# Kernel tuning notes

Measured on AMD Instinct MI355X. Metric: run time of the kernel, lower is better.

## Reference

```python
import jax, jax.numpy as jnp
import numpy as np

NUM_NODES = 10000  # fixed by input spec: edge_index values in [0, 10000)


def setup_inputs() -> dict:
    key = jax.random.key(0)
    k1, k2, k3 = jax.random.split(key, 3)
    N, E, D_IN, D_OUT = NUM_NODES, 320000, 256, 256
    x = jax.random.normal(k1, (N, D_IN), dtype=jnp.float32)
    edge_index = jax.random.randint(k2, (2, E), 0, N, dtype=jnp.int64)
    # ensure node N-1 appears so num_nodes == N as in the torch code
    edge_index = edge_index.at[0, 0].set(N - 1)
    # xavier_uniform for [D_IN, D_OUT]
    limit = float(np.sqrt(6.0 / (D_IN + D_OUT)))
    weight = jax.random.uniform(k3, (D_IN, D_OUT), dtype=jnp.float32,
                                minval=-limit, maxval=limit)
    return {"x": x, "edge_index": edge_index, "weight": weight}


def _normalize_adjacency(edge_index, num_nodes):
    src, dst = edge_index[0], edge_index[1]
    ones = jnp.ones(src.shape[0], dtype=jnp.float32)
    # symmetric binarized adjacency: adj[i,j] = adj[j,i] = 1 (set, not add)
    adj = jnp.zeros((num_nodes, num_nodes), dtype=jnp.float32)
    adj = adj.at[src, dst].max(ones)
    adj = adj.at[dst, src].max(ones)
    # one round of self-loops: adj += I
    adj = adj + jnp.eye(num_nodes, dtype=jnp.float32)
    deg = jnp.sum(adj, axis=1)                    # [N]
    dinv = 1.0 / jnp.sqrt(deg)                    # [N]
    # D^-1/2 A D^-1/2 via broadcasting (equivalent to diag mms)
    return adj * dinv[:, None] * dinv[None, :]


def reference(x, edge_index, weight):
    adj = _normalize_adjacency(edge_index, NUM_NODES)  # [N, N]
    h = adj @ x                                        # [N, D_IN]
    return h @ weight                                  # [N, D_OUT]
```

## Files before the change

### kernel.cpp

```cpp
#include <hip/hip_runtime.h>
#include <hip/hip_bf16.h>
#include <stdint.h>

#define N_NODES   10000
#define D_FEAT    256
#define E_EDGES   320000
#define ROW_WORDS 313
#define ROW_STRIDE 320
#define LIST_CAP  1024

#define NB     250
#define RPB    40
#define RPC    20
#define S_CAP  48
#define NBLK_E 313
#define NBLK_W 64
#define NBLK_C 500
#define NBLK_G 625
#define COLSTR 128

#define LDSTR 264

typedef __attribute__((ext_vector_type(4))) float float4v;
typedef _Float16 half8  __attribute__((ext_vector_type(8)));
typedef _Float16 half4v __attribute__((ext_vector_type(4)));

__device__ __forceinline__ float h2f_lo(uint32_t u) {
    union { uint32_t u; _Float16 h[2]; } v; v.u = u; return (float)v.h[0];
}
__device__ __forceinline__ float h2f_hi(uint32_t u) {
    union { uint32_t u; _Float16 h[2]; } v; v.u = u; return (float)v.h[1];
}


__global__ void __launch_bounds__(1024)
fill_sort(const int* __restrict__ ei, uint32_t* __restrict__ bucketbuf,
          uint32_t* __restrict__ hist_g,
          const float* __restrict__ w, _Float16* __restrict__ wt) {
    __shared__ uint32_t hist[256];
    __shared__ uint32_t lofs[256];
    __shared__ uint32_t stage[2048];
    __shared__ uint16_t sbkt[2048];
    int t = threadIdx.x;

    if (blockIdx.x >= NBLK_E) {
        int kb = (blockIdx.x - NBLK_E) * 4;
        int k = kb + (t >> 8), n = t & 255;
        float* st = (float*)stage;
        st[(n << 2) | (t >> 8)] = w[(size_t)k * D_FEAT + n];
        __syncthreads();
        if (t < 256) {
            half4v o = { (_Float16)st[t * 4 + 0], (_Float16)st[t * 4 + 1],
                         (_Float16)st[t * 4 + 2], (_Float16)st[t * 4 + 3] };
            *(half4v*)&wt[(size_t)t * D_FEAT + kb] = o;
        }
        return;
    }

    if (t < 256) hist[t] = 0;
    __syncthreads();
    int e = blockIdx.x * 1024 + t;
    int b0 = -1, b1 = -1; uint32_t ent0 = 0, ent1 = 0, s0 = 0, s1 = 0;
    if (e < E_EDGES) {
        int s = ei[e], d = ei[E_EDGES + e];
        if ((uint32_t)s < N_NODES && (uint32_t)d < N_NODES) {
            b0 = s / RPB; ent0 = ((uint32_t)(s - b0 * RPB) << 14) | (uint32_t)d;
            b1 = d / RPB; ent1 = ((uint32_t)(d - b1 * RPB) << 14) | (uint32_t)s;
            s0 = atomicAdd(&hist[b0], 1u);
            s1 = atomicAdd(&hist[b1], 1u);
        }
    }
    __syncthreads();
    if (t < 256) lofs[t] = hist[t];
    __syncthreads();
    for (int d = 1; d < 256; d <<= 1) {
        uint32_t v = 0;
        if (t < 256 && t >= d) v = lofs[t - d];
        __syncthreads();
        if (t < 256) lofs[t] += v;
        __syncthreads();
    }
    if (b0 >= 0) {
        uint32_t p0 = lofs[b0] - hist[b0] + s0;
        stage[p0] = ent0; sbkt[p0] = (uint16_t)b0;
        uint32_t p1 = lofs[b1] - hist[b1] + s1;
        stage[p1] = ent1; sbkt[p1] = (uint16_t)b1;
    }
    __syncthreads();
    uint32_t total = lofs[255];
    uint32_t bb0 = blockIdx.x * 256;
    for (uint32_t idx = t; idx < total; idx += 1024) {
        uint32_t b = sbkt[idx];
        uint32_t pos = idx - (lofs[b] - hist[b]);
        if (pos < S_CAP)
            bucketbuf[(size_t)(bb0 + b) * S_CAP + pos] = stage[idx];
    }
    if (t < 256) hist_g[bb0 + t] = min(hist[t], (uint32_t)S_CAP);
}

__global__ void __launch_bounds__(1024)
csr_gemm(const uint32_t* __restrict__ bucketbuf, const uint32_t* __restrict__ hist_g,
         uint32_t* __restrict__ row_deg, float* __restrict__ dinv,
         uint32_t* __restrict__ col,
         const float* __restrict__ x, const _Float16* __restrict__ wt,
         _Float16* __restrict__ yw) {
    __shared__ __align__(16) uint32_t smem[RPC * ROW_WORDS + NBLK_E];
    int t = threadIdx.x;

    if (blockIdx.x >= NBLK_C) {
        _Float16* a_lds = (_Float16*)smem;
        int r0 = (blockIdx.x - NBLK_C) * 16;
        int row = t >> 6, c4 = (t & 63) * 4;
        float4v xv = *(const float4v*)(x + (size_t)(r0 + row) * D_FEAT + c4);
        half4v h = { (_Float16)xv[0], (_Float16)xv[1],
                     (_Float16)xv[2], (_Float16)xv[3] };
        *(half4v*)&a_lds[row * LDSTR + c4] = h;
        __syncthreads();
        int wv = t >> 6, lane = t & 63;
        int quad = lane >> 4, r = lane & 15;
        int ct = wv;
        const _Float16* pb = wt + (size_t)(ct * 16 + r) * D_FEAT + quad * 8;
        float4v acc = {0.f, 0.f, 0.f, 0.f};
        #pragma unroll
        for (int kk = 0; kk < D_FEAT; kk += 32) {
            half8 a = *(const half8*)&a_lds[r * LDSTR + kk + quad * 8];
            half8 b = *(const half8*)(pb + kk);
            acc = __builtin_amdgcn_mfma_f32_16x16x32_f16(a, b, acc, 0, 0, 0);
        }
        int colg = ct * 16 + r;
        #pragma unroll
        for (int u = 0; u < 4; u++)
            yw[(size_t)(r0 + quad * 4 + u) * D_FEAT + colg] = (_Float16)acc[u];
        return;
    }

    uint32_t* bm       = smem;
    uint32_t* hist_col = smem + RPC * ROW_WORDS;
    int b   = blockIdx.x >> 1;
    int lr0 = (blockIdx.x & 1) * RPC;
    for (int i = t; i < RPC * ROW_WORDS; i += 1024) bm[i] = 0;
    if (t < NBLK_E) hist_col[t] = hist_g[(size_t)t * 256 + b];
    __syncthreads();
    for (int p = t; p < NBLK_E * S_CAP; p += 1024) {
        int sb = p / S_CAP, off = p % S_CAP;
        if ((uint32_t)off < hist_col[sb]) {
            uint32_t ent = bucketbuf[(size_t)(sb * 256 + b) * S_CAP + off];
            uint32_t lr = (ent >> 14) - (uint32_t)lr0;
            if (lr < RPC) {
                uint32_t d = ent & 0x3FFFu;
                atomicOr(&bm[lr * ROW_WORDS + (d >> 5)], 1u << (d & 31));
            }
        }
    }
    __syncthreads();
    int wv = t >> 6, lane = t & 63;
    for (int r = wv; r < RPC; r += 16) {
        int gi = b * RPB + lr0 + r;
        uint32_t wb[5]; int tot = 0;
        #pragma unroll
        for (int k = 0; k < 5; k++) {
            int w = lane + 64 * k;
            uint32_t v = (w < ROW_WORDS) ? bm[r * ROW_WORDS + w] : 0u;
            wb[k] = v; tot += __popc(v);
        }
        int incl = tot;
        #pragma unroll
        for (int off = 1; off < 64; off <<= 1) {
            int v = __shfl_up(incl, off, 64);
            if (lane >= off) incl += v;
        }
        uint32_t total = (uint32_t)__shfl(incl, 63, 64);
        if (lane == 0) {
            row_deg[gi] = min(total, (uint32_t)COLSTR);
            dinv[gi]    = 1.0f / sqrtf((float)(total + 1u));
        }
        uint32_t p = (uint32_t)(incl - tot);
        #pragma unroll
        for (int k = 0; k < 5; k++) {
            uint32_t bits = wb[k];
            uint32_t cbase = (uint32_t)(lane + 64 * k) << 5;
            while (bits) {
                if (p < COLSTR)
                    col[(size_t)gi * COLSTR + p] = cbase + (uint32_t)__builtin_ctz(bits);
                p++;
                bits &= bits - 1;
            }
        }
    }
}

__global__ void __launch_bounds__(256)
spmm_out(const uint32_t* __restrict__ row_deg, const float* __restrict__ dinv,
         const uint32_t* __restrict__ col, const _Float16* __restrict__ ywp,
         float* __restrict__ out) {
    const uint16_t* yw = (const uint16_t*)ywp;
    int wv = threadIdx.x >> 6, lane = threadIdx.x & 63;
    int i = blockIdx.x * 4 + wv;
    uint32_t base = (uint32_t)i * COLSTR;
    uint32_t deg = min(row_deg[i], (uint32_t)COLSTR);
    float di = dinv[i];
    float4v z = {0.f, 0.f, 0.f, 0.f};
    float4v a0 = z, a1 = z, a2 = z, a3 = z, a4 = z, a5 = z, a6 = z, a7 = z;
    size_t ch = (size_t)lane * 4;
    uint32_t t8 = deg & ~7u;
    uint32_t t = 0;
    for (; t < t8; t += 8) {
        uint4 jva = *(const uint4*)&col[base + t];
        uint4 jvb = *(const uint4*)&col[base + t + 4];
        float d0 = dinv[jva.x], d1 = dinv[jva.y], d2 = dinv[jva.z], d3 = dinv[jva.w];
        float d4 = dinv[jvb.x], d5 = dinv[jvb.y], d6 = dinv[jvb.z], d7 = dinv[jvb.w];
        uint2 g0 = *(const uint2*)(yw + (size_t)jva.x * D_FEAT + ch);
        uint2 g1 = *(const uint2*)(yw + (size_t)jva.y * D_FEAT + ch);
        uint2 g2 = *(const uint2*)(yw + (size_t)jva.z * D_FEAT + ch);
        uint2 g3 = *(const uint2*)(yw + (size_t)jva.w * D_FEAT + ch);
        uint2 g4 = *(const uint2*)(yw + (size_t)jvb.x * D_FEAT + ch);
        uint2 g5 = *(const uint2*)(yw + (size_t)jvb.y * D_FEAT + ch);
        uint2 g6 = *(const uint2*)(yw + (size_t)jvb.z * D_FEAT + ch);
        uint2 g7 = *(const uint2*)(yw + (size_t)jvb.w * D_FEAT + ch);
        a0[0] += d0 * h2f_lo(g0.x); a0[1] += d0 * h2f_hi(g0.x);
        a0[2] += d0 * h2f_lo(g0.y); a0[3] += d0 * h2f_hi(g0.y);
        a1[0] += d1 * h2f_lo(g1.x); a1[1] += d1 * h2f_hi(g1.x);
        a1[2] += d1 * h2f_lo(g1.y); a1[3] += d1 * h2f_hi(g1.y);
        a2[0] += d2 * h2f_lo(g2.x); a2[1] += d2 * h2f_hi(g2.x);
        a2[2] += d2 * h2f_lo(g2.y); a2[3] += d2 * h2f_hi(g2.y);
        a3[0] += d3 * h2f_lo(g3.x); a3[1] += d3 * h2f_hi(g3.x);
        a3[2] += d3 * h2f_lo(g3.y); a3[3] += d3 * h2f_hi(g3.y);
        a4[0] += d4 * h2f_lo(g4.x); a4[1] += d4 * h2f_hi(g4.x);
        a4[2] += d4 * h2f_lo(g4.y); a4[3] += d4 * h2f_hi(g4.y);
        a5[0] += d5 * h2f_lo(g5.x); a5[1] += d5 * h2f_hi(g5.x);
        a5[2] += d5 * h2f_lo(g5.y); a5[3] += d5 * h2f_hi(g5.y);
        a6[0] += d6 * h2f_lo(g6.x); a6[1] += d6 * h2f_hi(g6.x);
        a6[2] += d6 * h2f_lo(g6.y); a6[3] += d6 * h2f_hi(g6.y);
        a7[0] += d7 * h2f_lo(g7.x); a7[1] += d7 * h2f_hi(g7.x);
        a7[2] += d7 * h2f_lo(g7.y); a7[3] += d7 * h2f_hi(g7.y);
    }
    for (; t < deg; t++) {
        uint32_t j = col[base + t];
        float dj = dinv[j];
        uint2 g = *(const uint2*)(yw + (size_t)j * D_FEAT + ch);
        a0[0] += dj * h2f_lo(g.x); a0[1] += dj * h2f_hi(g.x);
        a0[2] += dj * h2f_lo(g.y); a0[3] += dj * h2f_hi(g.y);
    }
    uint2 gs = *(const uint2*)(yw + (size_t)i * D_FEAT + ch);
    a1[0] += di * h2f_lo(gs.x); a1[1] += di * h2f_hi(gs.x);
    a1[2] += di * h2f_lo(gs.y); a1[3] += di * h2f_hi(gs.y);
    float4v acc = ((a0 + a1) + (a2 + a3)) + ((a4 + a5) + (a6 + a7));
    *(float4v*)(out + (size_t)i * D_FEAT + ch) = di * acc;
}


__global__ void scatter_edges_fb(const int* __restrict__ ei,
                                 uint32_t* __restrict__ bitmap) {
    int e = blockIdx.x * blockDim.x + threadIdx.x;
    if (e >= E_EDGES) return;
    int s = ei[e], d = ei[E_EDGES + e];
    if ((uint32_t)s >= N_NODES || (uint32_t)d >= N_NODES) return;
    atomicOr(&bitmap[(size_t)s * ROW_STRIDE + (d >> 5)], 1u << (d & 31));
    atomicOr(&bitmap[(size_t)d * ROW_STRIDE + (s >> 5)], 1u << (s & 31));
}

__global__ void __launch_bounds__(256)
popc_dinv(const uint32_t* __restrict__ bitmap, float* __restrict__ dinv) {
    int wv = threadIdx.x >> 6, lane = threadIdx.x & 63;
    int i = blockIdx.x * 4 + wv;
    const uint32_t* rb = bitmap + (size_t)i * ROW_STRIDE;
    int pop = 0;
    #pragma unroll
    for (int k = 0; k < 5; k++) {
        int w = lane + 64 * k;
        if (w < ROW_WORDS) pop += __popc(rb[w]);
    }
    #pragma unroll
    for (int off = 32; off > 0; off >>= 1) pop += __shfl_xor(pop, off, 64);
    if (lane == 0) dinv[i] = 1.0f / sqrtf((float)(pop + 1));
}

__global__ void __launch_bounds__(256)
spmm_bitmap_fb(const uint32_t* __restrict__ bitmap, const float* __restrict__ dinv,
               const float* __restrict__ xf, float* __restrict__ agg) {
    __shared__ __align__(16) uint32_t lists[4][LIST_CAP];
    int wv = threadIdx.x >> 6, lane = threadIdx.x & 63;
    int i = blockIdx.x * 4 + wv;
    uint32_t* list = lists[wv];
    const uint32_t* rb = bitmap + (size_t)i * ROW_STRIDE;

    uint32_t wbits[5]; int tot = 0;
    #pragma unroll
    for (int k = 0; k < 5; k++) {
        int w = lane + 64 * k;
        uint32_t b = (w < ROW_WORDS) ? rb[w] : 0u;
        wbits[k] = b;
        tot += __popc(b);
    }
    int incl = tot;
    #pragma unroll
    for (int off = 1; off < 64; off <<= 1) {
        int v = __shfl_up(incl, off, 64);
        if (lane >= off) incl += v;
    }
    uint32_t p = (uint32_t)(incl - tot);
    uint32_t deg = (uint32_t)__shfl(incl, 63, 64);
    #pragma unroll
    for (int k = 0; k < 5; k++) {
        uint32_t bits = wbits[k];
        uint32_t base = (uint32_t)(lane + 64 * k) << 5;
        while (bits) {
            if (p < LIST_CAP) list[p] = base + (uint32_t)__builtin_ctz(bits);
            p++;
            bits &= bits - 1;
        }
    }
    if (deg > LIST_CAP) deg = LIST_CAP;

    float di = dinv[i];
    float4v z = {0.f, 0.f, 0.f, 0.f};
    float4v acc0 = z, acc1 = z, acc2 = z, acc3 = z;
    float4v sv = *(const float4v*)(xf + (size_t)i * D_FEAT + lane * 4);
    uint32_t t4 = deg & ~3u;
    for (uint32_t k = 0; k < t4; k += 4) {
        uint4 jv = *(const uint4*)&list[k];
        float d0 = dinv[jv.x], d1 = dinv[jv.y], d2 = dinv[jv.z], d3 = dinv[jv.w];
        float4v v0 = *(const float4v*)(xf + (size_t)jv.x * D_FEAT + lane * 4);
        float4v v1 = *(const float4v*)(xf + (size_t)jv.y * D_FEAT + lane * 4);
        float4v v2 = *(const float4v*)(xf + (size_t)jv.z * D_FEAT + lane * 4);
        float4v v3 = *(const float4v*)(xf + (size_t)jv.w * D_FEAT + lane * 4);
        acc0 += d0 * v0; acc1 += d1 * v1; acc2 += d2 * v2; acc3 += d3 * v3;
    }
    for (uint32_t k = t4; k < deg; k++) {
        uint32_t j = list[k];
        acc0 += dinv[j] * (*(const float4v*)(xf + (size_t)j * D_FEAT + lane * 4));
    }
    float4v acc = (acc0 + acc1) + (acc2 + acc3) + di * sv;
    *(float4v*)(agg + (size_t)i * D_FEAT + lane * 4) = di * acc;
}

__global__ void __launch_bounds__(256)
gemm_valu(float* __restrict__ io, const float* __restrict__ wf) {
    __shared__ __align__(16) float a_lds[16 * D_FEAT];
    int c = threadIdx.x;
    int r0 = blockIdx.x * 16;
    for (int idx = c; idx < 16 * D_FEAT; idx += 256)
        a_lds[idx] = io[(size_t)r0 * D_FEAT + idx];
    __syncthreads();
    float acc[16];
    #pragma unroll
    for (int r = 0; r < 16; r++) acc[r] = 0.f;
    for (int k0 = 0; k0 < D_FEAT; k0 += 4) {
        float w0 = wf[(size_t)(k0 + 0) * D_FEAT + c];
        float w1 = wf[(size_t)(k0 + 1) * D_FEAT + c];
        float w2 = wf[(size_t)(k0 + 2) * D_FEAT + c];
        float w3 = wf[(size_t)(k0 + 3) * D_FEAT + c];
        #pragma unroll
        for (int r = 0; r < 16; r++) {
            float4v av = *(const float4v*)&a_lds[r * D_FEAT + k0];
            acc[r] = fmaf(av[3], w3, fmaf(av[2], w2,
                     fmaf(av[1], w1, fmaf(av[0], w0, acc[r]))));
        }
    }
    #pragma unroll
    for (int r = 0; r < 16; r++)
        io[(size_t)(r0 + r) * D_FEAT + c] = acc[r];
}

extern "C" void kernel_launch(void* const* d_in, const int* in_sizes, int n_in,
                              void* d_out, int out_size, void* d_ws, size_t ws_size,
                              hipStream_t stream) {
    const float* x  = (const float*)d_in[0];
    const int*   ei = (const int*)d_in[1];
    const float* w  = (const float*)d_in[2];
    float* out = (float*)d_out;
    uint8_t* ws = (uint8_t*)d_ws;

    const size_t BB_OFF   = 320512;
    const size_t RD_OFF   = 15705088;
    const size_t DI_OFF   = 15745088;
    const size_t WT_OFF   = 15785088;
    const size_t YW_OFF   = 15916160;
    const size_t COL_OFF  = 21036160;
    const size_t NEED_NEW = 26156160;
    const size_t NEED_FB  = 12840000;

    if (ws_size >= NEED_NEW) {
        uint32_t* hist_g    = (uint32_t*)ws;
        uint32_t* bucketbuf = (uint32_t*)(ws + BB_OFF);
        uint32_t* row_deg   = (uint32_t*)(ws + RD_OFF);
        float*    dinv      = (float*)(ws + DI_OFF);
        _Float16* wt        = (_Float16*)(ws + WT_OFF);
        _Float16* yw        = (_Float16*)(ws + YW_OFF);
        uint32_t* col       = (uint32_t*)(ws + COL_OFF);

        fill_sort<<<NBLK_E + NBLK_W, 1024, 0, stream>>>(ei, bucketbuf, hist_g, w, wt);
        csr_gemm <<<NBLK_C + NBLK_G, 1024, 0, stream>>>(bucketbuf, hist_g,
                                                        row_deg, dinv, col, x, wt, yw);
        spmm_out <<<N_NODES / 4, 256, 0, stream>>>(row_deg, dinv, col, yw, out);
    } else if (ws_size >= NEED_FB) {
        uint32_t* bitmap = (uint32_t*)ws;
        float*    dinv   = (float*)(ws + 12800000);

        hipMemsetAsync(bitmap, 0, 12800000, stream);
        scatter_edges_fb<<<(E_EDGES + 255) / 256, 256, 0, stream>>>(ei, bitmap);
        popc_dinv      <<<N_NODES / 4, 256, 0, stream>>>(bitmap, dinv);
        spmm_bitmap_fb <<<N_NODES / 4, 256, 0, stream>>>(bitmap, dinv, x, out);
        gemm_valu      <<<N_NODES / 16, 256, 0, stream>>>(out, w);
    }
}
```

Baseline: 132.5 us.

## Replace per-block bucket slots with global atomic-cursor compact buckets

The edge sort now reserves space in one compact global bucket per 40-row group through an atomicAdd on a per-bucket cursor, replacing fixed 48-entry slots per (source block, bucket). The CSR-building blocks can then read a dense contiguous list instead of scanning 313x48 sparse slots, and each bucket is split across 4 blocks of 10 rows instead of 2 of 20. This removes wasted reads and the per-column histogram load. In exchange it adds a memset launch and global atomics, and each bucket is now read four times.

Measured after the change: 136.5 us. 3.0% more time.

```diff
diff --git a/kernel.cpp b/kernel.cpp
--- a/kernel.cpp
+++ b/kernel.cpp
@@ -11,11 +11,11 @@
 
 #define NB     250
 #define RPB    40
-#define RPC    20
-#define S_CAP  48
+#define B_CAP  8192
 #define NBLK_E 313
 #define NBLK_W 64
-#define NBLK_C 500
+#define RPC    10
+#define NBLK_C 1000
 #define NBLK_G 625
 #define COLSTR 128
 
@@ -34,11 +34,12 @@
 
 
 __global__ void __launch_bounds__(1024)
-fill_sort(const int* __restrict__ ei, uint32_t* __restrict__ bucketbuf,
-          uint32_t* __restrict__ hist_g,
-          const float* __restrict__ w, _Float16* __restrict__ wt) {
+fill_buckets(const int* __restrict__ ei, uint32_t* __restrict__ bucketbuf,
+             uint32_t* __restrict__ cursors,
+             const float* __restrict__ w, _Float16* __restrict__ wt) {
     __shared__ uint32_t hist[256];
     __shared__ uint32_t lofs[256];
+    __shared__ uint32_t base_s[256];
     __shared__ uint32_t stage[2048];
     __shared__ uint16_t sbkt[2048];
     int t = threadIdx.x;
@@ -80,6 +81,7 @@
         if (t < 256) lofs[t] += v;
         __syncthreads();
     }
+    if (t < 256) base_s[t] = hist[t] ? atomicAdd(&cursors[t], hist[t]) : 0u;
     if (b0 >= 0) {
         uint32_t p0 = lofs[b0] - hist[b0] + s0;
         stage[p0] = ent0; sbkt[p0] = (uint16_t)b0;
@@ -88,23 +90,20 @@
     }
     __syncthreads();
     uint32_t total = lofs[255];
-    uint32_t bb0 = blockIdx.x * 256;
     for (uint32_t idx = t; idx < total; idx += 1024) {
         uint32_t b = sbkt[idx];
-        uint32_t pos = idx - (lofs[b] - hist[b]);
-        if (pos < S_CAP)
-            bucketbuf[(size_t)(bb0 + b) * S_CAP + pos] = stage[idx];
-    }
-    if (t < 256) hist_g[bb0 + t] = min(hist[t], (uint32_t)S_CAP);
+        uint32_t pos = base_s[b] + (idx - (lofs[b] - hist[b]));
+        if (pos < B_CAP) bucketbuf[(size_t)b * B_CAP + pos] = stage[idx];
+    }
 }
 
 __global__ void __launch_bounds__(1024)
-csr_gemm(const uint32_t* __restrict__ bucketbuf, const uint32_t* __restrict__ hist_g,
+csr_gemm(const uint32_t* __restrict__ bucketbuf, const uint32_t* __restrict__ cursors,
          uint32_t* __restrict__ row_deg, float* __restrict__ dinv,
          uint32_t* __restrict__ col,
          const float* __restrict__ x, const _Float16* __restrict__ wt,
          _Float16* __restrict__ yw) {
-    __shared__ __align__(16) uint32_t smem[RPC * ROW_WORDS + NBLK_E];
+    __shared__ __align__(16) uint32_t smem[RPC * ROW_WORDS];
     int t = threadIdx.x;
 
     if (blockIdx.x >= NBLK_C) {
@@ -134,22 +133,19 @@
         return;
     }
 
-    uint32_t* bm       = smem;
-    uint32_t* hist_col = smem + RPC * ROW_WORDS;
-    int b   = blockIdx.x >> 1;
-    int lr0 = (blockIdx.x & 1) * RPC;
+    uint32_t* bm = smem;
+    int b   = blockIdx.x >> 2;
+    int lr0 = (blockIdx.x & 3) * RPC;
     for (int i = t; i < RPC * ROW_WORDS; i += 1024) bm[i] = 0;
-    if (t < NBLK_E) hist_col[t] = hist_g[(size_t)t * 256 + b];
-    __syncthreads();
-    for (int p = t; p < NBLK_E * S_CAP; p += 1024) {
-        int sb = p / S_CAP, off = p % S_CAP;
-        if ((uint32_t)off < hist_col[sb]) {
-            uint32_t ent = bucketbuf[(size_t)(sb * 256 + b) * S_CAP + off];
-            uint32_t lr = (ent >> 14) - (uint32_t)lr0;
-            if (lr < RPC) {
-                uint32_t d = ent & 0x3FFFu;
-                atomicOr(&bm[lr * ROW_WORDS + (d >> 5)], 1u << (d & 31));
-            }
+    __syncthreads();
+    uint32_t cnt = min(cursors[b], (uint32_t)B_CAP);
+    const uint32_t* bb = bucketbuf + (size_t)b * B_CAP;
+    for (uint32_t i = t; i < cnt; i += 1024) {
+        uint32_t ent = bb[i];
+        uint32_t lr = (ent >> 14) - (uint32_t)lr0;
+        if (lr < RPC) {
+            uint32_t d = ent & 0x3FFFu;
+            atomicOr(&bm[lr * ROW_WORDS + (d >> 5)], 1u << (d & 31));
         }
     }
     __syncthreads();
@@ -371,17 +367,17 @@
     float* out = (float*)d_out;
     uint8_t* ws = (uint8_t*)d_ws;
 
-    const size_t BB_OFF   = 320512;
-    const size_t RD_OFF   = 15705088;
-    const size_t DI_OFF   = 15745088;
-    const size_t WT_OFF   = 15785088;
-    const size_t YW_OFF   = 15916160;
-    const size_t COL_OFF  = 21036160;
-    const size_t NEED_NEW = 26156160;
+    const size_t BB_OFF   = 1024;
+    const size_t RD_OFF   = 8193024;
+    const size_t DI_OFF   = 8233024;
+    const size_t WT_OFF   = 8273024;
+    const size_t YW_OFF   = 8404096;
+    const size_t COL_OFF  = 13524096;
+    const size_t NEED_NEW = 18644096;
     const size_t NEED_FB  = 12840000;
 
     if (ws_size >= NEED_NEW) {
-        uint32_t* hist_g    = (uint32_t*)ws;
+        uint32_t* cursors   = (uint32_t*)ws;
         uint32_t* bucketbuf = (uint32_t*)(ws + BB_OFF);
         uint32_t* row_deg   = (uint32_t*)(ws + RD_OFF);
         float*    dinv      = (float*)(ws + DI_OFF);
@@ -389,10 +385,11 @@
         _Float16* yw        = (_Float16*)(ws + YW_OFF);
         uint32_t* col       = (uint32_t*)(ws + COL_OFF);
 
-        fill_sort<<<NBLK_E + NBLK_W, 1024, 0, stream>>>(ei, bucketbuf, hist_g, w, wt);
-        csr_gemm <<<NBLK_C + NBLK_G, 1024, 0, stream>>>(bucketbuf, hist_g,
-                                                        row_deg, dinv, col, x, wt, yw);
-        spmm_out <<<N_NODES / 4, 256, 0, stream>>>(row_deg, dinv, col, yw, out);
+        hipMemsetAsync(cursors, 0, 1024, stream);
+        fill_buckets<<<NBLK_E + NBLK_W, 1024, 0, stream>>>(ei, bucketbuf, cursors, w, wt);
+        csr_gemm    <<<NBLK_C + NBLK_G, 1024, 0, stream>>>(bucketbuf, cursors,
+                                                           row_deg, dinv, col, x, wt, yw);
+        spmm_out    <<<N_NODES / 4, 256, 0, stream>>>(row_deg, dinv, col, yw, out);
     } else if (ws_size >= NEED_FB) {
         uint32_t* bitmap = (uint32_t*)ws;
         float*    dinv   = (float*)(ws + 12800000);
```
